# Optimization experiments

Hardware: AMD Instinct MI355X
Metric: run time of the kernel (lower is better)

The kernel has to match this reference:

```python
import jax, jax.numpy as jnp
import numpy as np

NLAG = 300  # int(maxlag/dt) = int(3.0/0.01)


def setup_inputs() -> dict:
    key = jax.random.key(0)
    k1, k2 = jax.random.split(key)
    data1 = jax.random.normal(k1, (64, 32, 3000), dtype=jnp.float32)
    data2 = jax.random.normal(k2, (64, 32, 3000), dtype=jnp.float32)
    return {"data1": data1, "data2": data2}


def reference(data1, data2):
    # Time-domain full cross-correlation via grouped conv1d (PyTorch conv1d
    # does correlation, no kernel flip; lax.conv_general_dilated matches).
    nb, nc, nt = data1.shape
    g = nb * nc
    lhs = data1.reshape(1, g, nt)          # (N=1, C=g, T)
    rhs = data2.reshape(g, 1, nt)          # (O=g, I=1, T) one filter per group
    xcor = jax.lax.conv_general_dilated(
        lhs, rhs,
        window_strides=(1,),
        padding=[(NLAG + 1, NLAG + 1)],
        feature_group_count=g,
        dimension_numbers=("NCH", "OIH", "NCH"),
    )  # (1, g, 2*NLAG+3)
    return xcor.reshape(nb, nc, -1)
```

## Files before the change

kernel.cpp:

```cpp
#include <hip/hip_runtime.h>


#define NT    3000
#define NOUT  603
#define CHPB  2
#define BLOCK 256

#define L1B  6784
#define L2B  8192
#define CHB  (L1B + L2B)
#define TOTB (CHB * CHPB)

typedef short bf16x8 __attribute__((ext_vector_type(8)));
typedef float f32x4  __attribute__((ext_vector_type(4)));

static __device__ __forceinline__ uint f2bf(float f) {
    union { float f; uint u; } a; a.f = f;
    return (a.u + 0x7fffu + ((a.u >> 16) & 1u)) >> 16;
}

__global__ __launch_bounds__(BLOCK, 4) void xcorr_mfma(
    const float* __restrict__ d1g, const float* __restrict__ d2g,
    float* __restrict__ out)
{
    __shared__ __align__(16) unsigned char smem[TOTB];
    const int tid = threadIdx.x;
    const int chBase = blockIdx.x * CHPB;

    for (int i = tid; i < CHPB * 196; i += BLOCK) {
        const int c = i / 196, j = i % 196;
        const int dw = (j < 152) ? j : (1652 + (j - 152));
        ((uint*)(smem + c * CHB))[dw] = 0u;
    }
    for (int i = tid; i < CHPB * 548; i += BLOCK) {
        const int c = i / 548, j = i % 548;
        const int dw = (j < 384) ? j : (1884 + (j - 384));
        ((uint*)(smem + c * CHB + L1B))[dw] = 0u;
    }

    for (int i = tid; i < CHPB * 750; i += BLOCK) {
        const int c = i / 750, j = i % 750;
        const float4 v = *(const float4*)(d1g + (size_t)(chBase + c) * NT + 4 * j);
        uint2 p;
        p.x = f2bf(v.x) | (f2bf(v.y) << 16);
        p.y = f2bf(v.z) | (f2bf(v.w) << 16);
        *(uint2*)(smem + c * CHB + 608 + 8 * j) = p;
    }
    for (int i = tid; i < CHPB * 750; i += BLOCK) {
        const int c = i / 750, j = i % 750;
        const float4 v = *(const float4*)(d2g + (size_t)(chBase + c) * NT + 4 * j);
        uint2 p;
        p.x = f2bf(v.x) | (f2bf(v.y) << 16);
        p.y = f2bf(v.z) | (f2bf(v.w) << 16);
        *(uint2*)(smem + c * CHB + L1B + 1536 + 8 * j) = p;
    }
    __syncthreads();

    const int wid = tid >> 6, lane = tid & 63;
    const int c = wid >> 1, h = wid & 1;
    const int q = lane >> 4, r = lane & 15;
    const uint* lA = (const uint*)(smem + c * CHB);
    const uint* lB = (const uint*)(smem + c * CHB + L1B);

    f32x4 a00 = {0.f,0.f,0.f,0.f};
    f32x4 a10 = {0.f,0.f,0.f,0.f};
    f32x4 a01 = {0.f,0.f,0.f,0.f};
    f32x4 a11 = {0.f,0.f,0.f,0.f};

    int da = 130 + 4 * q + r + 768 * h;
    int db = 512 + 4 * q - 16 * r + 768 * h;

    #pragma unroll 4
    for (int i = 0; i < 48; ++i) {
        const uint* pa = lA + da;
        const uint Dm1 = pa[-1], D0 = pa[0], D1 = pa[1], D2 = pa[2], D3 = pa[3];

        union { uint w[4]; bf16x8 v; int4 i4; } f1, f0, g0, g1u;
        f1.w[0] = D0; f1.w[1] = D1; f1.w[2] = D2; f1.w[3] = D3;
        f0.w[0] = (Dm1 >> 16) | (D0 << 16);
        f0.w[1] = (D0  >> 16) | (D1 << 16);
        f0.w[2] = (D1  >> 16) | (D2 << 16);
        f0.w[3] = (D2  >> 16) | (D3 << 16);

        g0.i4  = *(const int4*)(lB + db);
        g1u.i4 = *(const int4*)(lB + db - 256);

        a00 = __builtin_amdgcn_mfma_f32_16x16x32_bf16(f0.v, g0.v,  a00, 0, 0, 0);
        a10 = __builtin_amdgcn_mfma_f32_16x16x32_bf16(f1.v, g0.v,  a10, 0, 0, 0);
        a01 = __builtin_amdgcn_mfma_f32_16x16x32_bf16(f0.v, g1u.v, a01, 0, 0, 0);
        a11 = __builtin_amdgcn_mfma_f32_16x16x32_bf16(f1.v, g1u.v, a11, 0, 0, 0);

        da += 16; db += 16;
    }

    __syncthreads();
    uint* S = (uint*)(smem + c * CHB);
    const int soff = lane * 17;
    if (h == 1) {
        *(f32x4*)(S + soff)      = a00;
        *(f32x4*)(S + soff + 4)  = a10;
        *(f32x4*)(S + soff + 8)  = a01;
        *(f32x4*)(S + soff + 12) = a11;
    }
    __syncthreads();
    if (h == 1) return;

    {
        const f32x4 b00 = *(const f32x4*)(S + soff);
        const f32x4 b10 = *(const f32x4*)(S + soff + 4);
        const f32x4 b01 = *(const f32x4*)(S + soff + 8);
        const f32x4 b11 = *(const f32x4*)(S + soff + 12);
        a00 += b00; a10 += b10; a01 += b01; a11 += b11;
    }

    float* o = out + (size_t)(chBase + c) * NOUT;
    {
        const int X = 32 * r + 8 * q;
        float4 s0 = {a00[0], a10[0], a00[1], a10[1]};
        float4 s1 = {a00[2], a10[2], a00[3], a10[3]};
        *(float4*)(o + X)     = s0;
        *(float4*)(o + X + 4) = s1;
    }
    {
        const int X = 512 + 32 * r + 8 * q;
        if (X + 7 < NOUT) {
            float4 s0 = {a01[0], a11[0], a01[1], a11[1]};
            float4 s1 = {a01[2], a11[2], a01[3], a11[3]};
            *(float4*)(o + X)     = s0;
            *(float4*)(o + X + 4) = s1;
        } else if (X < NOUT) {
            const float v[8] = {a01[0], a11[0], a01[1], a11[1],
                                a01[2], a11[2], a01[3], a11[3]};
            #pragma unroll
            for (int e = 0; e < 8; ++e)
                if (X + e < NOUT) o[X + e] = v[e];
        }
    }
}

extern "C" void kernel_launch(void* const* d_in, const int* in_sizes, int n_in,
                              void* d_out, int out_size, void* d_ws, size_t ws_size,
                              hipStream_t stream) {
    const float* d1 = (const float*)d_in[0];
    const float* d2 = (const float*)d_in[1];
    float* out = (float*)d_out;
    const int nChannels = in_sizes[0] / NT;
    const int grid = nChannels / CHPB;
    xcorr_mfma<<<grid, BLOCK, 0, stream>>>(d1, d2, out);
}
```

Before: 24.76 us.

## Use wave-private LDS staging and overlap global loads with MFMA chunks

The kernel now handles one channel per 128-thread block instead of two per 256-thread block. Each wave stages into LDS only the slice of data1/data2 it needs, so the block-wide barrier between staging and compute goes away. The later parts of the staging are issued as global loads before each 16-step MFMA chunk and packed to LDS after it, hiding load latency behind compute. The risk is that correctness now relies on in-order LDS access within a wave, and the extra boundary-predicated code adds instructions.

```diff
diff --git a/kernel.cpp b/kernel.cpp
--- a/kernel.cpp
+++ b/kernel.cpp
@@ -3,13 +3,10 @@
 
 #define NT    3000
 #define NOUT  603
-#define CHPB  2
-#define BLOCK 256
-
-#define L1B  6784
-#define L2B  8192
-#define CHB  (L1B + L2B)
-#define TOTB (CHB * CHPB)
+#define BLOCK 128
+#define PA_SZ 788
+#define PB_SZ 1264
+#define PW_SZ (PA_SZ + PB_SZ)
 
 typedef short bf16x8 __attribute__((ext_vector_type(8)));
 typedef float f32x4  __attribute__((ext_vector_type(4)));
@@ -17,86 +14,143 @@
 static __device__ __forceinline__ uint f2bf(float f) {
     union { float f; uint u; } a; a.f = f;
     return (a.u + 0x7fffu + ((a.u >> 16) & 1u)) >> 16;
+}
+
+static __device__ __forceinline__ int4 pack8(float4 v, float4 w) {
+    int4 p;
+    p.x = (int)(f2bf(v.x) | (f2bf(v.y) << 16));
+    p.y = (int)(f2bf(v.z) | (f2bf(v.w) << 16));
+    p.z = (int)(f2bf(w.x) | (f2bf(w.y) << 16));
+    p.w = (int)(f2bf(w.z) | (f2bf(w.w) << 16));
+    return p;
 }
 
 __global__ __launch_bounds__(BLOCK, 4) void xcorr_mfma(
     const float* __restrict__ d1g, const float* __restrict__ d2g,
     float* __restrict__ out)
 {
-    __shared__ __align__(16) unsigned char smem[TOTB];
-    const int tid = threadIdx.x;
-    const int chBase = blockIdx.x * CHPB;
-
-    for (int i = tid; i < CHPB * 196; i += BLOCK) {
-        const int c = i / 196, j = i % 196;
-        const int dw = (j < 152) ? j : (1652 + (j - 152));
-        ((uint*)(smem + c * CHB))[dw] = 0u;
-    }
-    for (int i = tid; i < CHPB * 548; i += BLOCK) {
-        const int c = i / 548, j = i % 548;
-        const int dw = (j < 384) ? j : (1884 + (j - 384));
-        ((uint*)(smem + c * CHB + L1B))[dw] = 0u;
-    }
-
-    for (int i = tid; i < CHPB * 750; i += BLOCK) {
-        const int c = i / 750, j = i % 750;
-        const float4 v = *(const float4*)(d1g + (size_t)(chBase + c) * NT + 4 * j);
-        uint2 p;
-        p.x = f2bf(v.x) | (f2bf(v.y) << 16);
-        p.y = f2bf(v.z) | (f2bf(v.w) << 16);
-        *(uint2*)(smem + c * CHB + 608 + 8 * j) = p;
-    }
-    for (int i = tid; i < CHPB * 750; i += BLOCK) {
-        const int c = i / 750, j = i % 750;
-        const float4 v = *(const float4*)(d2g + (size_t)(chBase + c) * NT + 4 * j);
-        uint2 p;
-        p.x = f2bf(v.x) | (f2bf(v.y) << 16);
-        p.y = f2bf(v.z) | (f2bf(v.w) << 16);
-        *(uint2*)(smem + c * CHB + L1B + 1536 + 8 * j) = p;
-    }
-    __syncthreads();
-
-    const int wid = tid >> 6, lane = tid & 63;
-    const int c = wid >> 1, h = wid & 1;
+    __shared__ __align__(16) uint smem[2 * PW_SZ];
+
+    const int tid  = threadIdx.x;
+    const int h    = tid >> 6;
+    const int lane = tid & 63;
     const int q = lane >> 4, r = lane & 15;
-    const uint* lA = (const uint*)(smem + c * CHB);
-    const uint* lB = (const uint*)(smem + c * CHB + L1B);
+    const int ch = blockIdx.x;
+    const float* __restrict__ g1 = d1g + (size_t)ch * NT;
+    const float* __restrict__ g2 = d2g + (size_t)ch * NT;
+
+    uint* pA = smem + h * PW_SZ;
+    uint* pB = pA + PA_SZ;
+    const int A0 = 128 + 768 * h;
+    const int B0 = 16  + 768 * h;
+
+    auto stageA = [&](int d) {
+        const int e0 = 2 * (A0 + d - 152);
+        int4 p = {0, 0, 0, 0};
+        if (0 <= e0 && e0 < NT)
+            p = pack8(*(const float4*)(g1 + e0), *(const float4*)(g1 + e0 + 4));
+        *(int4*)(pA + d) = p;
+    };
+    auto stageB = [&](int d) {
+        const int e0 = 2 * (B0 + d - 384);
+        int4 p = {0, 0, 0, 0};
+        if (0 <= e0 && e0 < NT)
+            p = pack8(*(const float4*)(g2 + e0), *(const float4*)(g2 + e0 + 4));
+        *(int4*)(pB + d) = p;
+    };
+
+    stageA(4 * lane);
+    stageA(256 + 4 * lane);
+    stageB(4 * lane);
+    stageB(256 + 4 * lane);
+    stageB(512 + 4 * lane);
 
     f32x4 a00 = {0.f,0.f,0.f,0.f};
     f32x4 a10 = {0.f,0.f,0.f,0.f};
     f32x4 a01 = {0.f,0.f,0.f,0.f};
     f32x4 a11 = {0.f,0.f,0.f,0.f};
 
-    int da = 130 + 4 * q + r + 768 * h;
-    int db = 512 + 4 * q - 16 * r + 768 * h;
-
-    #pragma unroll 4
-    for (int i = 0; i < 48; ++i) {
-        const uint* pa = lA + da;
-        const uint Dm1 = pa[-1], D0 = pa[0], D1 = pa[1], D2 = pa[2], D3 = pa[3];
-
-        union { uint w[4]; bf16x8 v; int4 i4; } f1, f0, g0, g1u;
-        f1.w[0] = D0; f1.w[1] = D1; f1.w[2] = D2; f1.w[3] = D3;
-        f0.w[0] = (Dm1 >> 16) | (D0 << 16);
-        f0.w[1] = (D0  >> 16) | (D1 << 16);
-        f0.w[2] = (D1  >> 16) | (D2 << 16);
-        f0.w[3] = (D2  >> 16) | (D3 << 16);
-
-        g0.i4  = *(const int4*)(lB + db);
-        g1u.i4 = *(const int4*)(lB + db - 256);
-
-        a00 = __builtin_amdgcn_mfma_f32_16x16x32_bf16(f0.v, g0.v,  a00, 0, 0, 0);
-        a10 = __builtin_amdgcn_mfma_f32_16x16x32_bf16(f1.v, g0.v,  a10, 0, 0, 0);
-        a01 = __builtin_amdgcn_mfma_f32_16x16x32_bf16(f0.v, g1u.v, a01, 0, 0, 0);
-        a11 = __builtin_amdgcn_mfma_f32_16x16x32_bf16(f1.v, g1u.v, a11, 0, 0, 0);
-
-        da += 16; db += 16;
-    }
-
-    __syncthreads();
-    uint* S = (uint*)(smem + c * CHB);
-    const int soff = lane * 17;
+    int da = 2 + 4 * q + r;
+    int db = 496 + 4 * q - 16 * r;
+
+    auto compute16 = [&]() {
+        #pragma unroll
+        for (int u = 0; u < 16; ++u) {
+            const uint* pa = pA + da;
+            const uint Dm1 = pa[-1], D0 = pa[0], D1 = pa[1], D2 = pa[2], D3 = pa[3];
+
+            union { uint w[4]; bf16x8 v; int4 i4; } f1, f0, gg0, gg1;
+            f1.w[0] = D0; f1.w[1] = D1; f1.w[2] = D2; f1.w[3] = D3;
+            f0.w[0] = (Dm1 >> 16) | (D0 << 16);
+            f0.w[1] = (D0  >> 16) | (D1 << 16);
+            f0.w[2] = (D1  >> 16) | (D2 << 16);
+            f0.w[3] = (D2  >> 16) | (D3 << 16);
+
+            gg0.i4 = *(const int4*)(pB + db);
+            gg1.i4 = *(const int4*)(pB + db - 256);
+
+            a00 = __builtin_amdgcn_mfma_f32_16x16x32_bf16(f0.v, gg0.v, a00, 0, 0, 0);
+            a10 = __builtin_amdgcn_mfma_f32_16x16x32_bf16(f1.v, gg0.v, a10, 0, 0, 0);
+            a01 = __builtin_amdgcn_mfma_f32_16x16x32_bf16(f0.v, gg1.v, a01, 0, 0, 0);
+            a11 = __builtin_amdgcn_mfma_f32_16x16x32_bf16(f1.v, gg1.v, a11, 0, 0, 0);
+
+            da += 16; db += 16;
+        }
+    };
+
+    {
+        const int dA2 = 512 + 4 * lane;
+        const int dA3 = 768 + 4 * lane;
+        const int dB3 = 768 + 4 * lane;
+        const int eA2 = 2 * (A0 + dA2 - 152);
+        const int eA3 = 2 * (A0 + dA3 - 152);
+        const int eB3 = 2 * (B0 + dB3 - 384);
+        const bool doA3 = dA3 < PA_SZ;
+        const bool okA2 = (0 <= eA2) && (eA2 < NT);
+        const bool okA3 = doA3 && (0 <= eA3) && (eA3 < NT);
+        const bool okB3 = (0 <= eB3) && (eB3 < NT);
+        float4 vA2a, vA2b, vA3a, vA3b, vB3a, vB3b;
+        if (okA2) { vA2a = *(const float4*)(g1 + eA2); vA2b = *(const float4*)(g1 + eA2 + 4); }
+        if (okA3) { vA3a = *(const float4*)(g1 + eA3); vA3b = *(const float4*)(g1 + eA3 + 4); }
+        if (okB3) { vB3a = *(const float4*)(g2 + eB3); vB3b = *(const float4*)(g2 + eB3 + 4); }
+
+        compute16();
+
+        int4 p = {0,0,0,0};
+        if (okA2) p = pack8(vA2a, vA2b);
+        *(int4*)(pA + dA2) = p;
+        if (doA3) {
+            int4 p3 = {0,0,0,0};
+            if (okA3) p3 = pack8(vA3a, vA3b);
+            *(int4*)(pA + dA3) = p3;
+        }
+        int4 pb3 = {0,0,0,0};
+        if (okB3) pb3 = pack8(vB3a, vB3b);
+        *(int4*)(pB + dB3) = pb3;
+    }
+
+    {
+        const int dB4 = 1024 + 4 * lane;
+        const int eB4 = 2 * (B0 + dB4 - 384);
+        const bool doB4 = dB4 < PB_SZ;
+        const bool okB4 = doB4 && (0 <= eB4) && (eB4 < NT);
+        float4 vB4a, vB4b;
+        if (okB4) { vB4a = *(const float4*)(g2 + eB4); vB4b = *(const float4*)(g2 + eB4 + 4); }
+
+        compute16();
+
+        if (doB4) {
+            int4 p = {0,0,0,0};
+            if (okB4) p = pack8(vB4a, vB4b);
+            *(int4*)(pB + dB4) = p;
+        }
+    }
+
+    compute16();
+
+    uint* S = smem + PW_SZ;
     if (h == 1) {
+        const int soff = lane * 20;
         *(f32x4*)(S + soff)      = a00;
         *(f32x4*)(S + soff + 4)  = a10;
         *(f32x4*)(S + soff + 8)  = a01;
@@ -106,14 +160,14 @@
     if (h == 1) return;
 
     {
-        const f32x4 b00 = *(const f32x4*)(S + soff);
-        const f32x4 b10 = *(const f32x4*)(S + soff + 4);
-        const f32x4 b01 = *(const f32x4*)(S + soff + 8);
-        const f32x4 b11 = *(const f32x4*)(S + soff + 12);
-        a00 += b00; a10 += b10; a01 += b01; a11 += b11;
-    }
-
-    float* o = out + (size_t)(chBase + c) * NOUT;
+        const int soff = lane * 20;
+        a00 += *(const f32x4*)(S + soff);
+        a10 += *(const f32x4*)(S + soff + 4);
+        a01 += *(const f32x4*)(S + soff + 8);
+        a11 += *(const f32x4*)(S + soff + 12);
+    }
+
+    float* o = out + (size_t)ch * NOUT;
     {
         const int X = 32 * r + 8 * q;
         float4 s0 = {a00[0], a10[0], a00[1], a10[1]};
@@ -145,6 +199,5 @@
     const float* d2 = (const float*)d_in[1];
     float* out = (float*)d_out;
     const int nChannels = in_sizes[0] / NT;
-    const int grid = nChannels / CHPB;
-    xcorr_mfma<<<grid, BLOCK, 0, stream>>>(d1, d2, out);
-}
+    xcorr_mfma<<<nChannels, BLOCK, 0, stream>>>(d1, d2, out);
+}
```

Result: faster. 23.95 us (-3.3%).
